# Kernel tuning notes

Hardware: AMD Instinct MI355X
Metric: run time of the kernel (lower is better)

The kernel has to match this reference:

```python
import jax, jax.numpy as jnp
import numpy as np

N = 10000
E = 160000
D_IN = 128
H = 1024
NUM_GRAPHS = 8
EPS = 1e-5


def setup_inputs() -> dict:
    key = jax.random.key(0)
    ks = jax.random.split(key, 24)
    x = jax.random.normal(ks[0], (N, D_IN), dtype=jnp.float32)
    edge_index = jax.random.randint(ks[1], (2, E), 0, N, dtype=jnp.int32)
    batch = jnp.sort(jax.random.randint(ks[2], (N,), 0, NUM_GRAPHS, dtype=jnp.int32))
    s = 0.02
    W1 = jax.random.normal(ks[3], (D_IN, H), dtype=jnp.float32) * s
    b1 = jnp.zeros((H,), jnp.float32)
    Wh = jax.random.normal(ks[4], (3, H, H), dtype=jnp.float32) * s
    bh = jnp.zeros((3, H), jnp.float32)
    ln_g = jnp.ones((4, H), jnp.float32)
    ln_b = jnp.zeros((4, H), jnp.float32)
    vW = jax.random.normal(ks[5], (6, H, H), dtype=jnp.float32) * s
    vb = jnp.zeros((6, H), jnp.float32)
    vWo = jax.random.normal(ks[6], (H, 1), dtype=jnp.float32) * s
    vbo = jnp.zeros((1,), jnp.float32)
    return {"x": x, "edge_index": edge_index, "batch": batch,
            "W1": W1, "b1": b1, "Wh": Wh, "bh": bh,
            "ln_g": ln_g, "ln_b": ln_b, "vW": vW, "vb": vb,
            "vWo": vWo, "vbo": vbo}


def _layer_norm(x, g, b):
    m = jnp.mean(x, axis=-1, keepdims=True)
    v = jnp.mean(jnp.square(x - m), axis=-1, keepdims=True)
    return (x - m) * jax.lax.rsqrt(v + EPS) * g + b


def reference(x, edge_index, batch, W1, b1, Wh, bh, ln_g, ln_b, vW, vb, vWo, vbo):
    # GCNConv: add self loops, symmetric normalization, x @ W, scatter-add at dst, + bias
    loops = jnp.arange(N, dtype=edge_index.dtype)
    src = jnp.concatenate([edge_index[0], loops])
    dst = jnp.concatenate([edge_index[1], loops])
    deg = jax.ops.segment_sum(jnp.ones_like(dst, dtype=x.dtype), dst, num_segments=N)
    dinv = jax.lax.rsqrt(jnp.maximum(deg, 1.0))
    norm = (dinv[src] * dinv[dst])[:, None]  # [E+N, 1]

    def gcn(h, W, b):
        h = h @ W                              # [N, H]
        msg = h[src] * norm                    # gather + scale [E+N, H]
        return jax.ops.segment_sum(msg, dst, num_segments=N) + b

    x1 = gcn(x, W1, b1)
    h = jax.nn.relu(_layer_norm(x1, ln_g[0], ln_b[0]))
    x2 = gcn(h, Wh[0], bh[0])
    h = jax.nn.relu(_layer_norm(x2 + x1, ln_g[1], ln_b[1]))
    x3 = gcn(h, Wh[1], bh[1])
    h = jax.nn.relu(_layer_norm(x3 + x1, ln_g[2], ln_b[2]))
    x4 = gcn(h, Wh[2], bh[2])
    node_embeddings = jax.nn.relu(_layer_norm(x4 + h, ln_g[3], ln_b[3]))

    # global mean pool per graph
    counts = jax.ops.segment_sum(jnp.ones((N,), x.dtype), batch, num_segments=NUM_GRAPHS)
    sums = jax.ops.segment_sum(node_embeddings, batch, num_segments=NUM_GRAPHS)
    graph_embedding = sums / jnp.maximum(counts, 1.0)[:, None]

    v = graph_embedding
    for i in range(6):
        v = jax.nn.relu(v @ vW[i] + vb[i])
    state_value = (v @ vWo + vbo).squeeze(-1)
    return node_embeddings, graph_embedding, state_value
```

## Files before the change

kernel.cpp:

```cpp
#include <hip/hip_runtime.h>
#include <stdint.h>

#define N_NODES 10000
#define E_EDGES 160000
#define DIN 128
#define H 1024
#define NUM_GRAPHS 8
#define LN_EPS 1e-5f

typedef unsigned short u16;
typedef __attribute__((ext_vector_type(8))) short short8;
typedef __attribute__((ext_vector_type(8))) unsigned short ushort8v;
typedef __attribute__((ext_vector_type(4))) float f32x4;

__device__ __forceinline__ float bf2f(u16 v) { return __uint_as_float(((unsigned)v) << 16); }
__device__ __forceinline__ u16 f2bf(float f) {
    unsigned u = __float_as_uint(f);
    u += 0x7fffu + ((u >> 16) & 1u);
    return (u16)(u >> 16);
}

__global__ void k_init(int* cnt, int* goff, float* __restrict__ gsum,
                       float* __restrict__ vbuf, const float* __restrict__ vb) {
    int i = blockIdx.x * 256 + threadIdx.x;
    if (i < N_NODES) cnt[i] = 0;
    if (i <= NUM_GRAPHS) goff[i] = 0;
    if (i < NUM_GRAPHS * H) gsum[i] = 0.f;
    if (i < 6 * H) {
        int il = i >> 10, j = i & (H - 1);
        float b = vb[il * H + j];
        float* base = vbuf + (size_t)(il + 1) * NUM_GRAPHS * H;
#pragma unroll
        for (int g = 0; g < NUM_GRAPHS; g++) base[g * H + j] = b;
    }
}

__global__ void k_count(const int* __restrict__ dst, int* __restrict__ cnt) {
    int e = blockIdx.x * 256 + threadIdx.x;
    if (e < E_EDGES) atomicAdd(&cnt[dst[e]], 1);
}

__global__ __launch_bounds__(1024) void k_scan(const int* __restrict__ cnt, int* __restrict__ offs,
                                               int* __restrict__ cursor, float* __restrict__ dinv) {
    __shared__ int s[1024];
    __shared__ int carry_s;
    int tid = threadIdx.x;
    if (tid == 0) carry_s = 0;
    __syncthreads();
    for (int base = 0; base < N_NODES; base += 1024) {
        int i = base + tid;
        int v = (i < N_NODES) ? cnt[i] : 0;
        s[tid] = v;
        __syncthreads();
        for (int off = 1; off < 1024; off <<= 1) {
            int t = (tid >= off) ? s[tid - off] : 0;
            __syncthreads();
            s[tid] += t;
            __syncthreads();
        }
        int incl = s[tid];
        int excl = incl - v;
        int cbase = carry_s;
        if (i < N_NODES) {
            offs[i] = cbase + excl;
            cursor[i] = cbase + excl;
            dinv[i] = rsqrtf((float)(v + 1));
        }
        __syncthreads();
        if (tid == 1023) carry_s = cbase + incl;
        __syncthreads();
    }
    if (tid == 0) offs[N_NODES] = carry_s;
}

__global__ void k_fill(const int* __restrict__ src, const int* __restrict__ dst,
                       int* __restrict__ cursor, int* __restrict__ csr_src) {
    int e = blockIdx.x * 256 + threadIdx.x;
    if (e < E_EDGES) {
        int d = dst[e];
        int slot = atomicAdd(&cursor[d], 1);
        csr_src[slot] = src[e];
    }
}

__global__ void k_gbound(const int* __restrict__ batch, int* __restrict__ goff) {
    int i = blockIdx.x * 256 + threadIdx.x;
    if (i >= N_NODES) return;
    int b0 = batch[i];
    int b1 = (i + 1 < N_NODES) ? batch[i + 1] : NUM_GRAPHS;
    for (int g = b0 + 1; g <= b1; g++) goff[g] = i + 1;
}

__global__ void k_cvt(const float* __restrict__ src, u16* __restrict__ dst, int n) {
    int i = blockIdx.x * 256 + threadIdx.x;
    if (i < n) dst[i] = f2bf(src[i]);
}

__global__ void k_transpose_cvt(const float* __restrict__ src, u16* __restrict__ dst, int R, int C) {
    __shared__ float tile[32][33];
    int tx = threadIdx.x, ty = threadIdx.y;
    int x = blockIdx.x * 32 + tx;
#pragma unroll
    for (int i = 0; i < 32; i += 8) {
        int y = blockIdx.y * 32 + ty + i;
        tile[ty + i][tx] = (y < R && x < C) ? src[(size_t)y * C + x] : 0.f;
    }
    __syncthreads();
    int xo = blockIdx.y * 32 + tx;
#pragma unroll
    for (int i = 0; i < 32; i += 8) {
        int yo = blockIdx.x * 32 + ty + i;
        if (yo < C && xo < R) dst[(size_t)yo * R + xo] = f2bf(tile[tx][ty + i]);
    }
}

typedef __attribute__((address_space(1))) const unsigned int gas_u32;
typedef __attribute__((address_space(3))) unsigned int las_u32;
__device__ __forceinline__ void gld_lds16(const void* g, void* l) {
    __builtin_amdgcn_global_load_lds((gas_u32*)g, (las_u32*)l, 16, 0, 0);
}

__global__ __launch_bounds__(256) void k_gemm(const u16* __restrict__ A, const u16* __restrict__ B,
                                              u16* __restrict__ C, int M, int Nn, int K) {
    __shared__ __align__(16) u16 sA[128 * 32];
    __shared__ __align__(16) u16 sB[128 * 32];
    int tid = threadIdx.x;
    int lane = tid & 63;
    int w = tid >> 6;
    int wm = w >> 1, wn = w & 1;
    int m0 = blockIdx.x * 128;
    int n0 = blockIdx.y * 128;

    f32x4 zero = {0.f, 0.f, 0.f, 0.f};
    f32x4 acc[4][4];
#pragma unroll
    for (int i = 0; i < 4; i++)
#pragma unroll
        for (int j = 0; j < 4; j++) acc[i][j] = zero;

    int srow = w * 32 + (lane >> 2);
    int scol = (lane & 3) * 8;
    u16* laA = sA + w * 1024;
    u16* laB = sB + w * 1024;

    for (int k0 = 0; k0 < K; k0 += 32) {
        __syncthreads();
#pragma unroll
        for (int q = 0; q < 2; q++) {
            int rA = m0 + srow + q * 16;
            rA = rA < M ? rA : M - 1;
            gld_lds16(A + (size_t)rA * K + k0 + scol, laA + q * 512);
            gld_lds16(B + (size_t)(n0 + srow + q * 16) * K + k0 + scol, laB + q * 512);
        }
        __syncthreads();

        short8 af[4], bv[4];
#pragma unroll
        for (int mi = 0; mi < 4; mi++)
            af[mi] = *(const short8*)(sA + (wm * 64 + mi * 16 + (lane & 15)) * 32 + (lane >> 4) * 8);
#pragma unroll
        for (int ni = 0; ni < 4; ni++)
            bv[ni] = *(const short8*)(sB + (wn * 64 + ni * 16 + (lane & 15)) * 32 + (lane >> 4) * 8);
#pragma unroll
        for (int mi = 0; mi < 4; mi++)
#pragma unroll
            for (int ni = 0; ni < 4; ni++)
                acc[mi][ni] = __builtin_amdgcn_mfma_f32_16x16x32_bf16(af[mi], bv[ni], acc[mi][ni], 0, 0, 0);
    }

    int rbase = m0 + wm * 64 + (lane >> 4) * 4;
    int cbase = n0 + wn * 64 + (lane & 15);
#pragma unroll
    for (int mi = 0; mi < 4; mi++) {
#pragma unroll
        for (int r = 0; r < 4; r++) {
            int row = rbase + mi * 16 + r;
            if (row < M) {
#pragma unroll
                for (int ni = 0; ni < 4; ni++)
                    C[(size_t)row * Nn + cbase + ni * 16] = f2bf(acc[mi][ni][r]);
            }
        }
    }
}

template <int MODE>
__global__ __launch_bounds__(128) void k_agg_ln(const u16* __restrict__ t, const u16* __restrict__ resid,
                                                const float* __restrict__ bias, const float* __restrict__ gamma,
                                                const float* __restrict__ beta, const float* __restrict__ dinv,
                                                const int* __restrict__ offs, const int* __restrict__ csr_src,
                                                u16* __restrict__ out_bf, u16* __restrict__ out_pre,
                                                float* __restrict__ out_f32) {
    __shared__ float s_dv[128];
    __shared__ int s_id[128];
    __shared__ float red1[2], red2[2];
    int d = blockIdx.x;
    int tid = threadIdx.x;
    int c = tid * 8;
    float dd = dinv[d];

    float a[8];
    {
        ushort8v v = *(const ushort8v*)(t + (size_t)d * H + c);
#pragma unroll
        for (int i = 0; i < 8; i++) a[i] = dd * bf2f(v[i]);
    }
    int beg = offs[d], end = offs[d + 1];
    for (int chunk = beg; chunk < end; chunk += 128) {
        int nthis = end - chunk;
        if (nthis > 128) nthis = 128;
        __syncthreads();
        if (tid < nthis) {
            int s = csr_src[chunk + tid];
            s_id[tid] = s;
            s_dv[tid] = dinv[s];
        }
        __syncthreads();
        for (int i = 0; i < nthis; i++) {
            int s = s_id[i];
            float ds = s_dv[i];
            ushort8v v = *(const ushort8v*)(t + (size_t)s * H + c);
#pragma unroll
            for (int j = 0; j < 8; j++) a[j] += ds * bf2f(v[j]);
        }
    }
    float x[8];
#pragma unroll
    for (int i = 0; i < 8; i++) x[i] = dd * a[i] + bias[c + i];
    if (MODE >= 1) {
        ushort8v r = *(const ushort8v*)(resid + (size_t)d * H + c);
#pragma unroll
        for (int i = 0; i < 8; i++) x[i] += bf2f(r[i]);
    }
    if (MODE == 0) {
        ushort8v p;
#pragma unroll
        for (int i = 0; i < 8; i++) p[i] = f2bf(x[i]);
        *(ushort8v*)(out_pre + (size_t)d * H + c) = p;
    }
    float s1 = 0.f, s2 = 0.f;
#pragma unroll
    for (int i = 0; i < 8; i++) { s1 += x[i]; s2 += x[i] * x[i]; }
#pragma unroll
    for (int off = 32; off > 0; off >>= 1) {
        s1 += __shfl_down(s1, off);
        s2 += __shfl_down(s2, off);
    }
    int lane = tid & 63, wv = tid >> 6;
    if (lane == 0) { red1[wv] = s1; red2[wv] = s2; }
    __syncthreads();
    float sum = red1[0] + red1[1];
    float ssq = red2[0] + red2[1];
    float mean = sum * (1.f / H);
    float var = fmaxf(ssq * (1.f / H) - mean * mean, 0.f);
    float inv = rsqrtf(var + LN_EPS);
    float y[8];
#pragma unroll
    for (int i = 0; i < 8; i++)
        y[i] = fmaxf((x[i] - mean) * inv * gamma[c + i] + beta[c + i], 0.f);
    if (MODE == 2) {
        float4 o0 = {y[0], y[1], y[2], y[3]};
        float4 o1 = {y[4], y[5], y[6], y[7]};
        *(float4*)(out_f32 + (size_t)d * H + c) = o0;
        *(float4*)(out_f32 + (size_t)d * H + c + 4) = o1;
    } else {
        ushort8v o;
#pragma unroll
        for (int i = 0; i < 8; i++) o[i] = f2bf(y[i]);
        *(ushort8v*)(out_bf + (size_t)d * H + c) = o;
    }
}

#define PC_NODES 16
__global__ __launch_bounds__(256) void k_pool_acc(const float* __restrict__ ne, const int* __restrict__ batch,
                                                  float* __restrict__ gsum) {
    int c = blockIdx.x * 256 + threadIdx.x;
    int nbeg = blockIdx.y * PC_NODES;
    int nend = nbeg + PC_NODES;
    if (nend > N_NODES) nend = N_NODES;
    float acc = 0.f;
    int curg = batch[nbeg];
    for (int n = nbeg; n < nend; n++) {
        int g = batch[n];
        if (g != curg) {
            atomicAdd(&gsum[curg * H + c], acc);
            acc = 0.f;
            curg = g;
        }
        acc += ne[(size_t)n * H + c];
    }
    atomicAdd(&gsum[curg * H + c], acc);
}

__global__ __launch_bounds__(256) void k_pool_fin(const float* __restrict__ gsum, const int* __restrict__ goff,
                                                  float* __restrict__ v0, float* __restrict__ ge_out) {
    int g = blockIdx.y;
    int c = blockIdx.x * 256 + threadIdx.x;
    float cntf = (float)(goff[g + 1] - goff[g]);
    float m = gsum[g * H + c] / fmaxf(cntf, 1.f);
    v0[g * H + c] = m;
    ge_out[(size_t)g * H + c] = m;
}

template <bool RELU_IN>
__global__ __launch_bounds__(256) void k_mlp_acc(const float* __restrict__ vin, const float* __restrict__ W,
                                                 float* __restrict__ vout) {
    __shared__ float sk[64];
    int g = blockIdx.y;
    int j = blockIdx.x * 256 + threadIdx.x;
    int k0 = blockIdx.z * 64;
    if (threadIdx.x < 64) {
        float v = vin[g * H + k0 + threadIdx.x];
        sk[threadIdx.x] = RELU_IN ? fmaxf(v, 0.f) : v;
    }
    __syncthreads();
    float acc = 0.f;
#pragma unroll
    for (int k = 0; k < 64; k++) acc += sk[k] * W[(size_t)(k0 + k) * H + j];
    atomicAdd(&vout[g * H + j], acc);
}

__global__ void k_head(const float* __restrict__ vin, const float* __restrict__ Wo,
                       const float* __restrict__ bo, float* __restrict__ out) {
    int g = blockIdx.x;
    int tid = threadIdx.x;
    float s = 0.f;
    for (int k = tid; k < H; k += 256) s += fmaxf(vin[g * H + k], 0.f) * Wo[k];
#pragma unroll
    for (int off = 32; off > 0; off >>= 1) s += __shfl_down(s, off);
    __shared__ float p[4];
    if ((tid & 63) == 0) p[tid >> 6] = s;
    __syncthreads();
    if (tid == 0) out[g] = p[0] + p[1] + p[2] + p[3] + bo[0];
}

extern "C" void kernel_launch(void* const* d_in, const int* in_sizes, int n_in,
                              void* d_out, int out_size, void* d_ws, size_t ws_size,
                              hipStream_t stream) {
    const float* x = (const float*)d_in[0];
    const int* ei = (const int*)d_in[1];
    const int* batch = (const int*)d_in[2];
    const float* W1 = (const float*)d_in[3];
    const float* b1 = (const float*)d_in[4];
    const float* Wh = (const float*)d_in[5];
    const float* bh = (const float*)d_in[6];
    const float* ln_g = (const float*)d_in[7];
    const float* ln_b = (const float*)d_in[8];
    const float* vW = (const float*)d_in[9];
    const float* vb = (const float*)d_in[10];
    const float* vWo = (const float*)d_in[11];
    const float* vbo = (const float*)d_in[12];
    const int* esrc = ei;
    const int* edst = ei + E_EDGES;

    char* ws = (char*)d_ws;
    size_t off = 0;
    auto carve = [&](size_t bytes) -> char* {
        char* p = ws + off;
        off += (bytes + 255) & ~(size_t)255;
        return p;
    };
    float* dinv = (float*)carve(N_NODES * 4);
    int* cnt = (int*)carve(N_NODES * 4);
    int* offs = (int*)carve((N_NODES + 1) * 4);
    int* cursor = (int*)carve(N_NODES * 4);
    int* csr_src = (int*)carve(E_EDGES * 4);
    int* goff = (int*)carve((NUM_GRAPHS + 1) * 4);
    float* gsum = (float*)carve(NUM_GRAPHS * H * 4);
    float* vbuf = (float*)carve((size_t)7 * NUM_GRAPHS * H * 4);
    u16* xb = (u16*)carve((size_t)N_NODES * DIN * 2);
    u16* Wt = (u16*)carve((size_t)H * H * 2);
    u16* tbuf = (u16*)carve((size_t)N_NODES * H * 2);
    u16* hbuf = (u16*)carve((size_t)N_NODES * H * 2);
    u16* x1buf = (u16*)carve((size_t)N_NODES * H * 2);

    float* out_ne = (float*)d_out;
    float* out_ge = out_ne + (size_t)N_NODES * H;
    float* out_sv = out_ge + (size_t)NUM_GRAPHS * H;

    k_init<<<(N_NODES + 255) / 256, 256, 0, stream>>>(cnt, goff, gsum, vbuf, vb);
    k_count<<<(E_EDGES + 255) / 256, 256, 0, stream>>>(edst, cnt);
    k_scan<<<1, 1024, 0, stream>>>(cnt, offs, cursor, dinv);
    k_fill<<<(E_EDGES + 255) / 256, 256, 0, stream>>>(esrc, edst, cursor, csr_src);
    k_gbound<<<(N_NODES + 255) / 256, 256, 0, stream>>>(batch, goff);
    k_cvt<<<(N_NODES * DIN + 255) / 256, 256, 0, stream>>>(x, xb, N_NODES * DIN);

    dim3 tb(32, 8);
    dim3 gg((N_NODES + 127) / 128, H / 128);

    k_transpose_cvt<<<dim3(H / 32, DIN / 32), tb, 0, stream>>>(W1, Wt, DIN, H);
    k_gemm<<<gg, 256, 0, stream>>>(xb, Wt, tbuf, N_NODES, H, DIN);
    k_agg_ln<0><<<N_NODES, 128, 0, stream>>>(tbuf, nullptr, b1, ln_g, ln_b, dinv, offs, csr_src,
                                             hbuf, x1buf, nullptr);

    k_transpose_cvt<<<dim3(H / 32, H / 32), tb, 0, stream>>>(Wh + 0 * (size_t)H * H, Wt, H, H);
    k_gemm<<<gg, 256, 0, stream>>>(hbuf, Wt, tbuf, N_NODES, H, H);
    k_agg_ln<1><<<N_NODES, 128, 0, stream>>>(tbuf, x1buf, bh, ln_g + H, ln_b + H, dinv, offs, csr_src,
                                             hbuf, nullptr, nullptr);

    k_transpose_cvt<<<dim3(H / 32, H / 32), tb, 0, stream>>>(Wh + 1 * (size_t)H * H, Wt, H, H);
    k_gemm<<<gg, 256, 0, stream>>>(hbuf, Wt, tbuf, N_NODES, H, H);
    k_agg_ln<1><<<N_NODES, 128, 0, stream>>>(tbuf, x1buf, bh + H, ln_g + 2 * H, ln_b + 2 * H, dinv, offs, csr_src,
                                             hbuf, nullptr, nullptr);

    k_transpose_cvt<<<dim3(H / 32, H / 32), tb, 0, stream>>>(Wh + 2 * (size_t)H * H, Wt, H, H);
    k_gemm<<<gg, 256, 0, stream>>>(hbuf, Wt, tbuf, N_NODES, H, H);
    k_agg_ln<2><<<N_NODES, 128, 0, stream>>>(tbuf, hbuf, bh + 2 * H, ln_g + 3 * H, ln_b + 3 * H, dinv, offs, csr_src,
                                             nullptr, nullptr, out_ne);

    k_pool_acc<<<dim3(H / 256, (N_NODES + PC_NODES - 1) / PC_NODES), 256, 0, stream>>>(out_ne, batch, gsum);
    k_pool_fin<<<dim3(H / 256, NUM_GRAPHS), 256, 0, stream>>>(gsum, goff, vbuf, out_ge);

    dim3 mg(H / 256, NUM_GRAPHS, 16);
    k_mlp_acc<false><<<mg, 256, 0, stream>>>(vbuf, vW, vbuf + (size_t)1 * NUM_GRAPHS * H);
    for (int i = 1; i < 6; i++)
        k_mlp_acc<true><<<mg, 256, 0, stream>>>(vbuf + (size_t)i * NUM_GRAPHS * H, vW + (size_t)i * H * H,
                                                vbuf + (size_t)(i + 1) * NUM_GRAPHS * H);
    k_head<<<NUM_GRAPHS, 256, 0, stream>>>(vbuf + (size_t)6 * NUM_GRAPHS * H, vWo, vbo, out_sv);
}
```

Before: 536.6 us.

## Split aggregation into column-sliced gather kernel and batch MLP over graphs

Aggregation is separated from LayerNorm. A new kernel gives each wave one destination node and one 128-column slice, so the grid is 8 slices by 2500 blocks. Each half-wave handles alternate neighbors with shuffle-broadcast indices instead of shared memory and syncthreads, and the partial sums are written to a bf16 buffer that a separate LN kernel reads. The MLP kernel now loads each weight once for all 8 graphs instead of once per graph, cutting weight traffic and atomics. The cost is an extra N×H bf16 round trip per layer, an extra bf16 rounding of the aggregate, and one more launch per layer.

New measurement: 617.8 us. 15.1% more time.

```diff
diff --git a/kernel.cpp b/kernel.cpp
--- a/kernel.cpp
+++ b/kernel.cpp
@@ -7,6 +7,8 @@
 #define H 1024
 #define NUM_GRAPHS 8
 #define LN_EPS 1e-5f
+#define SLICE_COLS 128
+#define SLICES (H / SLICE_COLS)
 
 typedef unsigned short u16;
 typedef __attribute__((ext_vector_type(8))) short short8;
@@ -184,49 +186,74 @@
     }
 }
 
+__global__ __launch_bounds__(256) void k_agg(const u16* __restrict__ t, const float* __restrict__ dinv,
+                                             const int* __restrict__ offs, const int* __restrict__ csr_src,
+                                             u16* __restrict__ xsum) {
+    int lane = threadIdx.x & 63;
+    int wv = threadIdx.x >> 6;
+    int d = blockIdx.y * 4 + wv;
+    int cbase = blockIdx.x * SLICE_COLS + (lane & 31) * 4;
+    int half = lane >> 5;
+
+    float a0 = 0.f, a1 = 0.f, a2 = 0.f, a3 = 0.f;
+    int beg = offs[d], end = offs[d + 1];
+    for (int chunk = beg; chunk < end; chunk += 64) {
+        int nthis = end - chunk;
+        if (nthis > 64) nthis = 64;
+        int rid = 0;
+        float rdv = 0.f;
+        if (lane < nthis) {
+            rid = csr_src[chunk + lane];
+            rdv = dinv[rid];
+        }
+        for (int i = 0; i < nthis; i += 2) {
+            int idx = i + half;
+            int s = __shfl(rid, idx);
+            float ds = __shfl(rdv, idx);
+            if (idx < nthis) {
+                ushort4 v = *(const ushort4*)(t + (size_t)s * H + cbase);
+                a0 += ds * bf2f(v.x);
+                a1 += ds * bf2f(v.y);
+                a2 += ds * bf2f(v.z);
+                a3 += ds * bf2f(v.w);
+            }
+        }
+    }
+    a0 += __shfl_down(a0, 32);
+    a1 += __shfl_down(a1, 32);
+    a2 += __shfl_down(a2, 32);
+    a3 += __shfl_down(a3, 32);
+    if (half == 0) {
+        float dd = dinv[d];
+        ushort4 v = *(const ushort4*)(t + (size_t)d * H + cbase);
+        a0 += dd * bf2f(v.x);
+        a1 += dd * bf2f(v.y);
+        a2 += dd * bf2f(v.z);
+        a3 += dd * bf2f(v.w);
+        ushort4 o;
+        o.x = f2bf(a0); o.y = f2bf(a1); o.z = f2bf(a2); o.w = f2bf(a3);
+        *(ushort4*)(xsum + (size_t)d * H + cbase) = o;
+    }
+}
+
 template <int MODE>
-__global__ __launch_bounds__(128) void k_agg_ln(const u16* __restrict__ t, const u16* __restrict__ resid,
-                                                const float* __restrict__ bias, const float* __restrict__ gamma,
-                                                const float* __restrict__ beta, const float* __restrict__ dinv,
-                                                const int* __restrict__ offs, const int* __restrict__ csr_src,
-                                                u16* __restrict__ out_bf, u16* __restrict__ out_pre,
-                                                float* __restrict__ out_f32) {
-    __shared__ float s_dv[128];
-    __shared__ int s_id[128];
+__global__ __launch_bounds__(128) void k_ln(const u16* __restrict__ xsum, const u16* __restrict__ resid,
+                                            const float* __restrict__ bias, const float* __restrict__ gamma,
+                                            const float* __restrict__ beta, const float* __restrict__ dinv,
+                                            u16* __restrict__ out_bf, u16* __restrict__ out_pre,
+                                            float* __restrict__ out_f32) {
     __shared__ float red1[2], red2[2];
     int d = blockIdx.x;
     int tid = threadIdx.x;
     int c = tid * 8;
     float dd = dinv[d];
 
-    float a[8];
+    float x[8];
     {
-        ushort8v v = *(const ushort8v*)(t + (size_t)d * H + c);
-#pragma unroll
-        for (int i = 0; i < 8; i++) a[i] = dd * bf2f(v[i]);
-    }
-    int beg = offs[d], end = offs[d + 1];
-    for (int chunk = beg; chunk < end; chunk += 128) {
-        int nthis = end - chunk;
-        if (nthis > 128) nthis = 128;
-        __syncthreads();
-        if (tid < nthis) {
-            int s = csr_src[chunk + tid];
-            s_id[tid] = s;
-            s_dv[tid] = dinv[s];
-        }
-        __syncthreads();
-        for (int i = 0; i < nthis; i++) {
-            int s = s_id[i];
-            float ds = s_dv[i];
-            ushort8v v = *(const ushort8v*)(t + (size_t)s * H + c);
-#pragma unroll
-            for (int j = 0; j < 8; j++) a[j] += ds * bf2f(v[j]);
-        }
-    }
-    float x[8];
-#pragma unroll
-    for (int i = 0; i < 8; i++) x[i] = dd * a[i] + bias[c + i];
+        ushort8v v = *(const ushort8v*)(xsum + (size_t)d * H + c);
+#pragma unroll
+        for (int i = 0; i < 8; i++) x[i] = dd * bf2f(v[i]) + bias[c + i];
+    }
     if (MODE >= 1) {
         ushort8v r = *(const ushort8v*)(resid + (size_t)d * H + c);
 #pragma unroll
@@ -305,19 +332,27 @@
 template <bool RELU_IN>
 __global__ __launch_bounds__(256) void k_mlp_acc(const float* __restrict__ vin, const float* __restrict__ W,
                                                  float* __restrict__ vout) {
-    __shared__ float sk[64];
-    int g = blockIdx.y;
+    __shared__ float sk[NUM_GRAPHS][64];
     int j = blockIdx.x * 256 + threadIdx.x;
-    int k0 = blockIdx.z * 64;
-    if (threadIdx.x < 64) {
-        float v = vin[g * H + k0 + threadIdx.x];
-        sk[threadIdx.x] = RELU_IN ? fmaxf(v, 0.f) : v;
+    int k0 = blockIdx.y * 64;
+    {
+        int g = threadIdx.x >> 6, kk = threadIdx.x & 63;
+        float v = vin[g * H + k0 + kk];
+        sk[g][kk] = RELU_IN ? fmaxf(v, 0.f) : v;
+        v = vin[(g + 4) * H + k0 + kk];
+        sk[g + 4][kk] = RELU_IN ? fmaxf(v, 0.f) : v;
     }
     __syncthreads();
-    float acc = 0.f;
-#pragma unroll
-    for (int k = 0; k < 64; k++) acc += sk[k] * W[(size_t)(k0 + k) * H + j];
-    atomicAdd(&vout[g * H + j], acc);
+    float acc[NUM_GRAPHS];
+#pragma unroll
+    for (int g = 0; g < NUM_GRAPHS; g++) acc[g] = 0.f;
+    for (int k = 0; k < 64; k++) {
+        float w = W[(size_t)(k0 + k) * H + j];
+#pragma unroll
+        for (int g = 0; g < NUM_GRAPHS; g++) acc[g] += sk[g][k] * w;
+    }
+#pragma unroll
+    for (int g = 0; g < NUM_GRAPHS; g++) atomicAdd(&vout[g * H + j], acc[g]);
 }
 
 __global__ void k_head(const float* __restrict__ vin, const float* __restrict__ Wo,
@@ -371,6 +406,7 @@
     u16* xb = (u16*)carve((size_t)N_NODES * DIN * 2);
     u16* Wt = (u16*)carve((size_t)H * H * 2);
     u16* tbuf = (u16*)carve((size_t)N_NODES * H * 2);
+    u16* xsum = (u16*)carve((size_t)N_NODES * H * 2);
     u16* hbuf = (u16*)carve((size_t)N_NODES * H * 2);
     u16* x1buf = (u16*)carve((size_t)N_NODES * H * 2);
 
@@ -387,31 +423,33 @@
 
     dim3 tb(32, 8);
     dim3 gg((N_NODES + 127) / 128, H / 128);
+    dim3 ag(SLICES, N_NODES / 4);
 
     k_transpose_cvt<<<dim3(H / 32, DIN / 32), tb, 0, stream>>>(W1, Wt, DIN, H);
     k_gemm<<<gg, 256, 0, stream>>>(xb, Wt, tbuf, N_NODES, H, DIN);
-    k_agg_ln<0><<<N_NODES, 128, 0, stream>>>(tbuf, nullptr, b1, ln_g, ln_b, dinv, offs, csr_src,
-                                             hbuf, x1buf, nullptr);
+    k_agg<<<ag, 256, 0, stream>>>(tbuf, dinv, offs, csr_src, xsum);
+    k_ln<0><<<N_NODES, 128, 0, stream>>>(xsum, nullptr, b1, ln_g, ln_b, dinv, hbuf, x1buf, nullptr);
 
     k_transpose_cvt<<<dim3(H / 32, H / 32), tb, 0, stream>>>(Wh + 0 * (size_t)H * H, Wt, H, H);
     k_gemm<<<gg, 256, 0, stream>>>(hbuf, Wt, tbuf, N_NODES, H, H);
-    k_agg_ln<1><<<N_NODES, 128, 0, stream>>>(tbuf, x1buf, bh, ln_g + H, ln_b + H, dinv, offs, csr_src,
-                                             hbuf, nullptr, nullptr);
+    k_agg<<<ag, 256, 0, stream>>>(tbuf, dinv, offs, csr_src, xsum);
+    k_ln<1><<<N_NODES, 128, 0, stream>>>(xsum, x1buf, bh, ln_g + H, ln_b + H, dinv, hbuf, nullptr, nullptr);
 
     k_transpose_cvt<<<dim3(H / 32, H / 32), tb, 0, stream>>>(Wh + 1 * (size_t)H * H, Wt, H, H);
     k_gemm<<<gg, 256, 0, stream>>>(hbuf, Wt, tbuf, N_NODES, H, H);
-    k_agg_ln<1><<<N_NODES, 128, 0, stream>>>(tbuf, x1buf, bh + H, ln_g + 2 * H, ln_b + 2 * H, dinv, offs, csr_src,
-                                             hbuf, nullptr, nullptr);
+    k_agg<<<ag, 256, 0, stream>>>(tbuf, dinv, offs, csr_src, xsum);
+    k_ln<1><<<N_NODES, 128, 0, stream>>>(xsum, x1buf, bh + H, ln_g + 2 * H, ln_b + 2 * H, dinv, hbuf, nullptr, nullptr);
 
     k_transpose_cvt<<<dim3(H / 32, H / 32), tb, 0, stream>>>(Wh + 2 * (size_t)H * H, Wt, H, H);
     k_gemm<<<gg, 256, 0, stream>>>(hbuf, Wt, tbuf, N_NODES, H, H);
-    k_agg_ln<2><<<N_NODES, 128, 0, stream>>>(tbuf, hbuf, bh + 2 * H, ln_g + 3 * H, ln_b + 3 * H, dinv, offs, csr_src,
-                                             nullptr, nullptr, out_ne);
+    k_agg<<<ag, 256, 0, stream>>>(tbuf, dinv, offs, csr_src, xsum);
+    k_ln<2><<<N_NODES, 128, 0, stream>>>(xsum, hbuf, bh + 2 * H, ln_g + 3 * H, ln_b + 3 * H, dinv,
+                                         nullptr, nullptr, out_ne);
 
     k_pool_acc<<<dim3(H / 256, (N_NODES + PC_NODES - 1) / PC_NODES), 256, 0, stream>>>(out_ne, batch, gsum);
     k_pool_fin<<<dim3(H / 256, NUM_GRAPHS), 256, 0, stream>>>(gsum, goff, vbuf, out_ge);
 
-    dim3 mg(H / 256, NUM_GRAPHS, 16);
+    dim3 mg(H / 256, 16);
     k_mlp_acc<false><<<mg, 256, 0, stream>>>(vbuf, vW, vbuf + (size_t)1 * NUM_GRAPHS * H);
     for (int i = 1; i < 6; i++)
         k_mlp_acc<true><<<mg, 256, 0, stream>>>(vbuf + (size_t)i * NUM_GRAPHS * H, vW + (size_t)i * H * H,
```

## Split fused aggregation+LayerNorm into column-sliced gather kernel and separate LN kernel

Applied to the files above, without the earlier changes.

Splits the per-node aggregate-and-LayerNorm kernel into two kernels. The first gathers neighbour rows in 128-column slices, one wavefront per node, with 4-way unrolled independent loads and two accumulators, and writes a bf16 partial sum. The second applies bias, residual and LayerNorm. The goal is better L2 locality, since each column slice of the gathered matrix is small enough to stay cached, and more memory-level parallelism. The cost is an extra N×H bf16 round trip, an extra launch per layer, and an extra bf16 rounding of the aggregate before LayerNorm.

Result: slower. 571.7 us (+6.5%).

```diff
diff --git a/kernel.cpp b/kernel.cpp
--- a/kernel.cpp
+++ b/kernel.cpp
@@ -7,6 +7,8 @@
 #define H 1024
 #define NUM_GRAPHS 8
 #define LN_EPS 1e-5f
+#define SLICE_COLS 128
+#define SLICES (H / SLICE_COLS)
 
 typedef unsigned short u16;
 typedef __attribute__((ext_vector_type(8))) short short8;
@@ -184,49 +186,63 @@
     }
 }
 
+__global__ __launch_bounds__(256) void k_agg(const u16* __restrict__ t, const float* __restrict__ dinv,
+                                             const int* __restrict__ offs, const int* __restrict__ csr_src,
+                                             u16* __restrict__ xsum) {
+    int lane = threadIdx.x & 63;
+    int wv = threadIdx.x >> 6;
+    int d = blockIdx.y * 4 + wv;
+    int cbase = blockIdx.x * SLICE_COLS + lane * 2;
+    const u16* tp = t + cbase;
+
+    float a0 = 0.f, a1 = 0.f, b0 = 0.f, b1 = 0.f;
+    int beg = offs[d], end = offs[d + 1];
+    int i = beg;
+    for (; i + 4 <= end; i += 4) {
+        int s0 = csr_src[i], s1 = csr_src[i + 1], s2 = csr_src[i + 2], s3 = csr_src[i + 3];
+        float e0 = dinv[s0], e1 = dinv[s1], e2 = dinv[s2], e3 = dinv[s3];
+        ushort2 v0 = *(const ushort2*)(tp + (size_t)s0 * H);
+        ushort2 v1 = *(const ushort2*)(tp + (size_t)s1 * H);
+        ushort2 v2 = *(const ushort2*)(tp + (size_t)s2 * H);
+        ushort2 v3 = *(const ushort2*)(tp + (size_t)s3 * H);
+        a0 += e0 * bf2f(v0.x); a1 += e0 * bf2f(v0.y);
+        b0 += e1 * bf2f(v1.x); b1 += e1 * bf2f(v1.y);
+        a0 += e2 * bf2f(v2.x); a1 += e2 * bf2f(v2.y);
+        b0 += e3 * bf2f(v3.x); b1 += e3 * bf2f(v3.y);
+    }
+    for (; i < end; i++) {
+        int s = csr_src[i];
+        float ds = dinv[s];
+        ushort2 v = *(const ushort2*)(tp + (size_t)s * H);
+        a0 += ds * bf2f(v.x); a1 += ds * bf2f(v.y);
+    }
+    float dd = dinv[d];
+    ushort2 v = *(const ushort2*)(tp + (size_t)d * H);
+    a0 += b0 + dd * bf2f(v.x);
+    a1 += b1 + dd * bf2f(v.y);
+    ushort2 o;
+    o.x = f2bf(a0); o.y = f2bf(a1);
+    *(ushort2*)(xsum + (size_t)d * H + cbase) = o;
+}
+
 template <int MODE>
-__global__ __launch_bounds__(128) void k_agg_ln(const u16* __restrict__ t, const u16* __restrict__ resid,
-                                                const float* __restrict__ bias, const float* __restrict__ gamma,
-                                                const float* __restrict__ beta, const float* __restrict__ dinv,
-                                                const int* __restrict__ offs, const int* __restrict__ csr_src,
-                                                u16* __restrict__ out_bf, u16* __restrict__ out_pre,
-                                                float* __restrict__ out_f32) {
-    __shared__ float s_dv[128];
-    __shared__ int s_id[128];
+__global__ __launch_bounds__(128) void k_ln(const u16* __restrict__ xsum, const u16* __restrict__ resid,
+                                            const float* __restrict__ bias, const float* __restrict__ gamma,
+                                            const float* __restrict__ beta, const float* __restrict__ dinv,
+                                            u16* __restrict__ out_bf, u16* __restrict__ out_pre,
+                                            float* __restrict__ out_f32) {
     __shared__ float red1[2], red2[2];
     int d = blockIdx.x;
     int tid = threadIdx.x;
     int c = tid * 8;
     float dd = dinv[d];
 
-    float a[8];
+    float x[8];
     {
-        ushort8v v = *(const ushort8v*)(t + (size_t)d * H + c);
-#pragma unroll
-        for (int i = 0; i < 8; i++) a[i] = dd * bf2f(v[i]);
-    }
-    int beg = offs[d], end = offs[d + 1];
-    for (int chunk = beg; chunk < end; chunk += 128) {
-        int nthis = end - chunk;
-        if (nthis > 128) nthis = 128;
-        __syncthreads();
-        if (tid < nthis) {
-            int s = csr_src[chunk + tid];
-            s_id[tid] = s;
-            s_dv[tid] = dinv[s];
-        }
-        __syncthreads();
-        for (int i = 0; i < nthis; i++) {
-            int s = s_id[i];
-            float ds = s_dv[i];
-            ushort8v v = *(const ushort8v*)(t + (size_t)s * H + c);
-#pragma unroll
-            for (int j = 0; j < 8; j++) a[j] += ds * bf2f(v[j]);
-        }
-    }
-    float x[8];
-#pragma unroll
-    for (int i = 0; i < 8; i++) x[i] = dd * a[i] + bias[c + i];
+        ushort8v v = *(const ushort8v*)(xsum + (size_t)d * H + c);
+#pragma unroll
+        for (int i = 0; i < 8; i++) x[i] = dd * bf2f(v[i]) + bias[c + i];
+    }
     if (MODE >= 1) {
         ushort8v r = *(const ushort8v*)(resid + (size_t)d * H + c);
 #pragma unroll
@@ -371,6 +387,7 @@
     u16* xb = (u16*)carve((size_t)N_NODES * DIN * 2);
     u16* Wt = (u16*)carve((size_t)H * H * 2);
     u16* tbuf = (u16*)carve((size_t)N_NODES * H * 2);
+    u16* xsum = (u16*)carve((size_t)N_NODES * H * 2);
     u16* hbuf = (u16*)carve((size_t)N_NODES * H * 2);
     u16* x1buf = (u16*)carve((size_t)N_NODES * H * 2);
 
@@ -387,26 +404,28 @@
 
     dim3 tb(32, 8);
     dim3 gg((N_NODES + 127) / 128, H / 128);
+    dim3 ag(SLICES, N_NODES / 4);
 
     k_transpose_cvt<<<dim3(H / 32, DIN / 32), tb, 0, stream>>>(W1, Wt, DIN, H);
     k_gemm<<<gg, 256, 0, stream>>>(xb, Wt, tbuf, N_NODES, H, DIN);
-    k_agg_ln<0><<<N_NODES, 128, 0, stream>>>(tbuf, nullptr, b1, ln_g, ln_b, dinv, offs, csr_src,
-                                             hbuf, x1buf, nullptr);
+    k_agg<<<ag, 256, 0, stream>>>(tbuf, dinv, offs, csr_src, xsum);
+    k_ln<0><<<N_NODES, 128, 0, stream>>>(xsum, nullptr, b1, ln_g, ln_b, dinv, hbuf, x1buf, nullptr);
 
     k_transpose_cvt<<<dim3(H / 32, H / 32), tb, 0, stream>>>(Wh + 0 * (size_t)H * H, Wt, H, H);
     k_gemm<<<gg, 256, 0, stream>>>(hbuf, Wt, tbuf, N_NODES, H, H);
-    k_agg_ln<1><<<N_NODES, 128, 0, stream>>>(tbuf, x1buf, bh, ln_g + H, ln_b + H, dinv, offs, csr_src,
-                                             hbuf, nullptr, nullptr);
+    k_agg<<<ag, 256, 0, stream>>>(tbuf, dinv, offs, csr_src, xsum);
+    k_ln<1><<<N_NODES, 128, 0, stream>>>(xsum, x1buf, bh, ln_g + H, ln_b + H, dinv, hbuf, nullptr, nullptr);
 
     k_transpose_cvt<<<dim3(H / 32, H / 32), tb, 0, stream>>>(Wh + 1 * (size_t)H * H, Wt, H, H);
     k_gemm<<<gg, 256, 0, stream>>>(hbuf, Wt, tbuf, N_NODES, H, H);
-    k_agg_ln<1><<<N_NODES, 128, 0, stream>>>(tbuf, x1buf, bh + H, ln_g + 2 * H, ln_b + 2 * H, dinv, offs, csr_src,
-                                             hbuf, nullptr, nullptr);
+    k_agg<<<ag, 256, 0, stream>>>(tbuf, dinv, offs, csr_src, xsum);
+    k_ln<1><<<N_NODES, 128, 0, stream>>>(xsum, x1buf, bh + H, ln_g + 2 * H, ln_b + 2 * H, dinv, hbuf, nullptr, nullptr);
 
     k_transpose_cvt<<<dim3(H / 32, H / 32), tb, 0, stream>>>(Wh + 2 * (size_t)H * H, Wt, H, H);
     k_gemm<<<gg, 256, 0, stream>>>(hbuf, Wt, tbuf, N_NODES, H, H);
-    k_agg_ln<2><<<N_NODES, 128, 0, stream>>>(tbuf, hbuf, bh + 2 * H, ln_g + 3 * H, ln_b + 3 * H, dinv, offs, csr_src,
-                                             nullptr, nullptr, out_ne);
+    k_agg<<<ag, 256, 0, stream>>>(tbuf, dinv, offs, csr_src, xsum);
+    k_ln<2><<<N_NODES, 128, 0, stream>>>(xsum, hbuf, bh + 2 * H, ln_g + 3 * H, ln_b + 3 * H, dinv,
+                                         nullptr, nullptr, out_ne);
 
     k_pool_acc<<<dim3(H / 256, (N_NODES + PC_NODES - 1) / PC_NODES), 256, 0, stream>>>(out_ne, batch, gsum);
     k_pool_fin<<<dim3(H / 256, NUM_GRAPHS), 256, 0, stream>>>(gsum, goff, vbuf, out_ge);
```
